# Optimization experiments

Hardware: AMD Instinct MI355X
Metric: run time of the kernel (lower is better)

Reference implementation:

```python
import jax, jax.numpy as jnp
import numpy as np

BN_EPS = 1e-5


def gcn_conv(x, src, dst, n, W, b):
    # PyG GCNConv: h = x @ W; add self-loops; symmetric deg^{-1/2} norm; scatter-add; + bias
    h = x @ W
    sl = jnp.arange(n, dtype=src.dtype)
    src_f = jnp.concatenate([src, sl])
    dst_f = jnp.concatenate([dst, sl])
    deg = jax.ops.segment_sum(jnp.ones_like(dst_f, dtype=h.dtype), dst_f, num_segments=n)
    dis = jnp.where(deg > 0, jax.lax.rsqrt(jnp.maximum(deg, 1.0)), 0.0)
    norm = dis[src_f] * dis[dst_f]                       # [E+N]
    msg = h[src_f] * norm[:, None]                       # gather + scale
    out = jax.ops.segment_sum(msg, dst_f, num_segments=n)  # scatter-add
    return out + b


def batchnorm(x, g, b):
    # training-mode BatchNorm1d (batch statistics), deterministic
    mu = jnp.mean(x, axis=0)
    var = jnp.mean((x - mu) ** 2, axis=0)
    return g * (x - mu) * jax.lax.rsqrt(var + BN_EPS) + b


def setup_inputs() -> dict:
    key = jax.random.key(0)
    ks = jax.random.split(key, 12)
    N, E, F_IN, D, M, G = 40000, 640000, 128, 128, 256, 2000
    x = jax.random.normal(ks[0], (N, F_IN), dtype=jnp.float32)
    edge_index = jax.random.randint(ks[1], (2, E), 0, N, dtype=jnp.int64)
    batch = jnp.sort(jax.random.randint(ks[2], (N,), 0, G, dtype=jnp.int64))
    s = lambda fi: 1.0 / np.sqrt(fi)
    W1 = jax.random.normal(ks[3], (F_IN, D), dtype=jnp.float32) * s(F_IN)
    b1 = jnp.zeros((D,), jnp.float32)
    W2 = jax.random.normal(ks[4], (D, D), dtype=jnp.float32) * s(D)
    b2 = jnp.zeros((D,), jnp.float32)
    bn1_g = jnp.ones((D,), jnp.float32); bn1_b = jnp.zeros((D,), jnp.float32)
    bn2_g = jnp.ones((D,), jnp.float32); bn2_b = jnp.zeros((D,), jnp.float32)
    fc1_w = jax.random.normal(ks[5], (D, M), dtype=jnp.float32) * s(D)
    fc1_b = jnp.zeros((M,), jnp.float32)
    fc2_w = jax.random.normal(ks[6], (M, M), dtype=jnp.float32) * s(M)
    fc2_b = jnp.zeros((M,), jnp.float32)
    fc3_w = jax.random.normal(ks[7], (M, 1), dtype=jnp.float32) * s(M)
    fc3_b = jnp.zeros((1,), jnp.float32)
    return dict(x=x, edge_index=edge_index, batch=batch, num_graphs=G,
                W1=W1, b1=b1, W2=W2, b2=b2,
                bn1_g=bn1_g, bn1_b=bn1_b, bn2_g=bn2_g, bn2_b=bn2_b,
                fc1_w=fc1_w, fc1_b=fc1_b, fc2_w=fc2_w, fc2_b=fc2_b,
                fc3_w=fc3_w, fc3_b=fc3_b)


def reference(x, edge_index, batch, num_graphs, W1, b1, W2, b2,
              bn1_g, bn1_b, bn2_g, bn2_b,
              fc1_w, fc1_b, fc2_w, fc2_b, fc3_w, fc3_b):
    n = x.shape[0]
    src, dst = edge_index[0], edge_index[1]
    h = gcn_conv(x, src, dst, n, W1, b1)
    h = jax.nn.relu(batchnorm(h, bn1_g, bn1_b))
    h = gcn_conv(h, src, dst, n, W2, b2)
    h = jax.nn.relu(batchnorm(h, bn2_g, bn2_b))
    g = jax.ops.segment_sum(h, batch, num_segments=num_graphs)  # scatter_sum pooling [G, D]
    g = jax.nn.relu(g @ fc1_w + fc1_b)   # dropout is identity in eval
    g = jax.nn.relu(g @ fc2_w + fc2_b)
    return g @ fc3_w + fc3_b             # [G, 1]
```

## Files before the change

kernel.cpp:

```cpp
#include <hip/hip_runtime.h>

#define NN 40000
#define NE 640000
#define DF 128
#define NG 2000
#define NCH 157
#define FILLB 625
#define GEMM_BLKS 313

typedef unsigned int u32;
typedef __attribute__((ext_vector_type(8))) short short8;
typedef __attribute__((ext_vector_type(4))) float floatx4;

__device__ inline float2 bf2_to_f2(u32 u) {
    return make_float2(__uint_as_float(u << 16), __uint_as_float(u & 0xffff0000u));
}
__device__ inline u32 f_to_bf(float f) {
    u32 u = __float_as_uint(f);
    return (u + 0x7fffu + ((u >> 16) & 1u)) >> 16;
}
__device__ inline u32 pack_bf2(float a, float b) {
    return f_to_bf(a) | (f_to_bf(b) << 16);
}
__device__ inline float bf_to_f(short s) {
    return __uint_as_float(((u32)(unsigned short)s) << 16);
}

template<bool BF16IN, bool FUSE_BN, bool WT_F32>
__device__ __forceinline__ void gemm_core(const void* __restrict__ Xv, const void* __restrict__ wsrc,
                                          u32* __restrict__ outb, const float* __restrict__ slots,
                                          const float* __restrict__ gam, const float* __restrict__ bet, int bid) {
    __shared__ unsigned short uni[128 * 136];
    __shared__ float sc[128], sh[128];
    unsigned short* wlds = uni;
    unsigned short* clds = uni;
    int tid = threadIdx.x;
    int row0 = bid * 128;

    if (FUSE_BN) {
        if (tid < 128) {
            float s = 0.f, q = 0.f;
            for (int k = 0; k < 64; k++) {
                s += slots[k * 256 + tid];
                q += slots[k * 256 + 128 + tid];
            }
            const float inv_n = 1.0f / (float)NN;
            float mu = s * inv_n;
            float va = fmaf(-mu, mu, q * inv_n);
            float a = gam[tid] * rsqrtf(va + 1e-5f);
            sc[tid] = a;
            sh[tid] = fmaf(-mu, a, bet[tid]);
        }
    }
    if (WT_F32) {
        const float* W = (const float*)wsrc;
        for (int i = tid; i < 16384; i += 256) {
            int k = i >> 7, c = i & 127;
            wlds[c * 136 + k] = (unsigned short)f_to_bf(W[i]);
        }
    } else {
        const unsigned short* wt = (const unsigned short*)wsrc;
        for (int i = tid; i < 2048; i += 256) {
            int c = i >> 4, s = i & 15;
            *(uint4*)&wlds[c * 136 + s * 8] = ((const uint4*)wt)[i];
        }
    }
    __syncthreads();

    int lane = tid & 63;
    int wave = tid >> 6;
    int qr = lane >> 4;
    int rl = lane & 15;
    int rA0 = row0 + wave * 32 + rl;
    int rA1 = rA0 + 16;
    int rA0c = rA0 < NN ? rA0 : NN - 1;
    int rA1c = rA1 < NN ? rA1 : NN - 1;

    floatx4 acc[2][8];
#pragma unroll
    for (int a = 0; a < 2; a++)
#pragma unroll
        for (int b = 0; b < 8; b++) acc[a][b] = (floatx4){0.f, 0.f, 0.f, 0.f};

#pragma unroll
    for (int kb = 0; kb < 4; kb++) {
        int k0 = kb * 32 + qr * 8;
        short8 a0, a1;
        if (!BF16IN) {
            const float* p0 = (const float*)Xv + (size_t)rA0c * DF + k0;
            const float* p1 = (const float*)Xv + (size_t)rA1c * DF + k0;
            float4 u0 = *(const float4*)p0, u1 = *(const float4*)(p0 + 4);
            float4 v0 = *(const float4*)p1, v1 = *(const float4*)(p1 + 4);
            float fa[8] = {u0.x, u0.y, u0.z, u0.w, u1.x, u1.y, u1.z, u1.w};
            float fb[8] = {v0.x, v0.y, v0.z, v0.w, v1.x, v1.y, v1.z, v1.w};
#pragma unroll
            for (int j = 0; j < 8; j++) { a0[j] = (short)f_to_bf(fa[j]); a1[j] = (short)f_to_bf(fb[j]); }
        } else {
            a0 = *(const short8*)((const u32*)Xv + (size_t)rA0c * 64 + (k0 >> 1));
            a1 = *(const short8*)((const u32*)Xv + (size_t)rA1c * 64 + (k0 >> 1));
            if (FUSE_BN) {
                float4 s0 = *(const float4*)&sc[k0], s1 = *(const float4*)&sc[k0 + 4];
                float4 h0 = *(const float4*)&sh[k0], h1 = *(const float4*)&sh[k0 + 4];
                float ss[8] = {s0.x, s0.y, s0.z, s0.w, s1.x, s1.y, s1.z, s1.w};
                float hh[8] = {h0.x, h0.y, h0.z, h0.w, h1.x, h1.y, h1.z, h1.w};
#pragma unroll
                for (int j = 0; j < 8; j++) {
                    float f0 = fmaxf(fmaf(bf_to_f(a0[j]), ss[j], hh[j]), 0.f);
                    float f1 = fmaxf(fmaf(bf_to_f(a1[j]), ss[j], hh[j]), 0.f);
                    a0[j] = (short)f_to_bf(f0);
                    a1[j] = (short)f_to_bf(f1);
                }
            }
        }
#pragma unroll
        for (int ct = 0; ct < 8; ct++) {
            short8 bfr = *(const short8*)&wlds[(ct * 16 + rl) * 136 + k0];
            acc[0][ct] = __builtin_amdgcn_mfma_f32_16x16x32_bf16(a0, bfr, acc[0][ct], 0, 0, 0);
            acc[1][ct] = __builtin_amdgcn_mfma_f32_16x16x32_bf16(a1, bfr, acc[1][ct], 0, 0, 0);
        }
    }
    __syncthreads();
#pragma unroll
    for (int rt = 0; rt < 2; rt++)
#pragma unroll
        for (int ct = 0; ct < 8; ct++)
#pragma unroll
            for (int r = 0; r < 4; r++) {
                int lr = wave * 32 + rt * 16 + qr * 4 + r;
                int c = ct * 16 + rl;
                clds[lr * 136 + c] = (unsigned short)f_to_bf(acc[rt][ct][r]);
            }
    __syncthreads();
    for (int i = tid; i < 2048; i += 256) {
        int lr = i >> 4, s = i & 15;
        int grow = row0 + lr;
        if (grow < NN) {
            uint4 v = *(const uint4*)&clds[lr * 136 + s * 8];
            ((uint4*)(outb + (size_t)grow * 64))[s] = v;
        }
    }
}

__global__ __launch_bounds__(256, 4) void k_countgemm(const int* __restrict__ dst, int* __restrict__ deg,
                                                      const float* __restrict__ W1, const float* __restrict__ W2,
                                                      unsigned short* __restrict__ wt2,
                                                      const float* __restrict__ X, u32* __restrict__ outb) {
    int bid = blockIdx.x;
    if (bid < FILLB) {
        int e0 = bid * 1024 + threadIdx.x;
        int d0 = dst[e0], d1 = dst[e0 + 256], d2 = dst[e0 + 512], d3 = dst[e0 + 768];
        atomicAdd(&deg[d0], 1);
        atomicAdd(&deg[d1], 1);
        atomicAdd(&deg[d2], 1);
        atomicAdd(&deg[d3], 1);
        return;
    }
    if (bid == FILLB) {
        for (int i = threadIdx.x; i < 128 * 128; i += 256) {
            int k = i >> 7, c = i & 127;
            wt2[c * 128 + k] = (unsigned short)f_to_bf(W2[i]);
        }
        return;
    }
    gemm_core<false, false, true>(X, W1, outb, nullptr, nullptr, nullptr, bid - FILLB - 1);
}

__global__ __launch_bounds__(256) void k_scan(const int* __restrict__ deg,
                                              int* __restrict__ row_ptr, int* __restrict__ cursor,
                                              float* __restrict__ dis) {
    __shared__ int red[256];
    __shared__ int ls[256];
    int tid = threadIdx.x;
    int blk = blockIdx.x;
    int limit = blk * 256;
    int partial = 0;
    for (int i = tid; i < limit; i += 256) partial += deg[i];
    red[tid] = partial;
    int i = limit + tid;
    int d = (i < NN) ? deg[i] : 0;
    ls[tid] = d;
    __syncthreads();
#pragma unroll
    for (int off = 128; off > 0; off >>= 1) {
        if (tid < off) red[tid] += red[tid + off];
        __syncthreads();
    }
    int base = red[0];
#pragma unroll
    for (int off = 1; off < 256; off <<= 1) {
        int t = (tid >= off) ? ls[tid - off] : 0;
        __syncthreads();
        ls[tid] += t;
        __syncthreads();
    }
    if (i < NN) {
        int r = base + ls[tid] - d;
        row_ptr[i] = r;
        cursor[i] = r;
        dis[i] = rsqrtf((float)(d + 1));
    }
    if (blk == NCH - 1 && tid == 0) row_ptr[NN] = NE;
}

__global__ __launch_bounds__(256) void k_fill(const int* __restrict__ src, const int* __restrict__ dst,
                                              int* __restrict__ cursor, int* __restrict__ col) {
    int e0 = blockIdx.x * 1024 + threadIdx.x;
    int d0 = dst[e0], d1 = dst[e0 + 256], d2 = dst[e0 + 512], d3 = dst[e0 + 768];
    int s0 = src[e0], s1 = src[e0 + 256], s2 = src[e0 + 512], s3 = src[e0 + 768];
    int p0 = atomicAdd(&cursor[d0], 1);
    int p1 = atomicAdd(&cursor[d1], 1);
    int p2 = atomicAdd(&cursor[d2], 1);
    int p3 = atomicAdd(&cursor[d3], 1);
    col[p0] = s0;
    col[p1] = s1;
    col[p2] = s2;
    col[p3] = s3;
}

__global__ __launch_bounds__(256, 4) void k_gemm2(const u32* __restrict__ Hb, const unsigned short* __restrict__ wt2,
                                                  u32* __restrict__ outb, const float* __restrict__ slots,
                                                  const float* __restrict__ gam, const float* __restrict__ bet) {
    gemm_core<true, true, false>(Hb, wt2, outb, slots, gam, bet, blockIdx.x);
}

__global__ __launch_bounds__(256) void k_gather(const u32* __restrict__ Hb, const int* __restrict__ row_ptr,
                                                const int* __restrict__ col, const float* __restrict__ dis,
                                                const float* __restrict__ bias, u32* __restrict__ outb,
                                                float* __restrict__ slots) {
    __shared__ float sred[4][128];
    __shared__ float qred[4][128];
    int t = threadIdx.x & 63;
    int wv = threadIdx.x >> 6;
    int node = blockIdx.x * 4 + wv;
    float di = dis[node];
    float2 acc;
    {
        float2 a = bf2_to_f2(Hb[(size_t)node * 64 + t]);
        float s = di * di;
        acc = make_float2(a.x * s, a.y * s);
    }
    int lo = row_ptr[node], hi = row_ptr[node + 1];
    for (int base = lo; base < hi; base += 64) {
        int m = hi - base; if (m > 64) m = 64;
        int sidx = 0; float sw = 0.f;
        if (t < m) { sidx = col[base + t]; sw = di * dis[sidx]; }
        int j = 0;
        for (; j + 8 <= m; j += 8) {
            int s0 = __shfl(sidx, j),     s1 = __shfl(sidx, j + 1);
            int s2 = __shfl(sidx, j + 2), s3 = __shfl(sidx, j + 3);
            int s4 = __shfl(sidx, j + 4), s5 = __shfl(sidx, j + 5);
            int s6 = __shfl(sidx, j + 6), s7 = __shfl(sidx, j + 7);
            float w0 = __shfl(sw, j),     w1 = __shfl(sw, j + 1);
            float w2 = __shfl(sw, j + 2), w3 = __shfl(sw, j + 3);
            float w4 = __shfl(sw, j + 4), w5 = __shfl(sw, j + 5);
            float w6 = __shfl(sw, j + 6), w7 = __shfl(sw, j + 7);
            u32 u0 = Hb[(size_t)s0 * 64 + t], u1 = Hb[(size_t)s1 * 64 + t];
            u32 u2 = Hb[(size_t)s2 * 64 + t], u3 = Hb[(size_t)s3 * 64 + t];
            u32 u4 = Hb[(size_t)s4 * 64 + t], u5 = Hb[(size_t)s5 * 64 + t];
            u32 u6 = Hb[(size_t)s6 * 64 + t], u7 = Hb[(size_t)s7 * 64 + t];
            float2 h0 = bf2_to_f2(u0), h1 = bf2_to_f2(u1), h2 = bf2_to_f2(u2), h3 = bf2_to_f2(u3);
            float2 h4 = bf2_to_f2(u4), h5 = bf2_to_f2(u5), h6 = bf2_to_f2(u6), h7 = bf2_to_f2(u7);
            acc.x = fmaf(h3.x, w3, fmaf(h2.x, w2, fmaf(h1.x, w1, fmaf(h0.x, w0, acc.x))));
            acc.y = fmaf(h3.y, w3, fmaf(h2.y, w2, fmaf(h1.y, w1, fmaf(h0.y, w0, acc.y))));
            acc.x = fmaf(h7.x, w7, fmaf(h6.x, w6, fmaf(h5.x, w5, fmaf(h4.x, w4, acc.x))));
            acc.y = fmaf(h7.y, w7, fmaf(h6.y, w6, fmaf(h5.y, w5, fmaf(h4.y, w4, acc.y))));
        }
        for (; j < m; j++) {
            int s0 = __shfl(sidx, j); float w0 = __shfl(sw, j);
            float2 h0 = bf2_to_f2(Hb[(size_t)s0 * 64 + t]);
            acc.x = fmaf(h0.x, w0, acc.x);
            acc.y = fmaf(h0.y, w0, acc.y);
        }
    }
    float2 b = ((const float2*)bias)[t];
    acc.x += b.x; acc.y += b.y;
    outb[(size_t)node * 64 + t] = pack_bf2(acc.x, acc.y);
    sred[wv][2 * t] = acc.x;     sred[wv][2 * t + 1] = acc.y;
    qred[wv][2 * t] = acc.x * acc.x; qred[wv][2 * t + 1] = acc.y * acc.y;
    __syncthreads();
    int tid = threadIdx.x;
    if (tid < 128) {
        float s = sred[0][tid] + sred[1][tid] + sred[2][tid] + sred[3][tid];
        float q = qred[0][tid] + qred[1][tid] + qred[2][tid] + qred[3][tid];
        int slot = blockIdx.x & 63;
        atomicAdd(&slots[slot * 256 + tid], s);
        atomicAdd(&slots[slot * 256 + 128 + tid], q);
    }
}

__global__ __launch_bounds__(256) void k_poolfc(const u32* __restrict__ Hb, const int* __restrict__ batch,
                                                const float* __restrict__ slots,
                                                const float* __restrict__ gam, const float* __restrict__ bet,
                                                const float* __restrict__ fc1w, const float* __restrict__ fc1b,
                                                const float* __restrict__ fc2w, const float* __restrict__ fc2b,
                                                const float* __restrict__ fc3w, const float* __restrict__ fc3b,
                                                float* __restrict__ out) {
    __shared__ float sc[128], sh[128];
    __shared__ float pooled[4][128];
    __shared__ float g1[4][256];
    __shared__ float g2[4][256];
    __shared__ int bnds[5];
    int tid = threadIdx.x;
    int gbase = blockIdx.x * 4;
    if (tid < 128) {
        float s = 0.f, q = 0.f;
        for (int k = 0; k < 64; k++) {
            s += slots[k * 256 + tid];
            q += slots[k * 256 + 128 + tid];
        }
        const float inv_n = 1.0f / (float)NN;
        float mu = s * inv_n;
        float va = fmaf(-mu, mu, q * inv_n);
        float a = gam[tid] * rsqrtf(va + 1e-5f);
        sc[tid] = a;
        sh[tid] = fmaf(-mu, a, bet[tid]);
    } else if (tid < 133) {
        int target = gbase + (tid - 128);
        int a = 0, b = NN;
        while (a < b) { int m = (a + b) >> 1; if (batch[m] < target) a = m + 1; else b = m; }
        bnds[tid - 128] = a;
    }
    __syncthreads();
    {
        int g = tid >> 6, p = tid & 63;
        int lo = bnds[g], hi = bnds[g + 1];
        float a0 = 0.f, a1 = 0.f;
        float sc0 = sc[2 * p], sh0 = sh[2 * p], sc1 = sc[2 * p + 1], sh1 = sh[2 * p + 1];
        for (int i = lo; i < hi; i++) {
            float2 v = bf2_to_f2(Hb[(size_t)i * 64 + p]);
            a0 += fmaxf(fmaf(v.x, sc0, sh0), 0.f);
            a1 += fmaxf(fmaf(v.y, sc1, sh1), 0.f);
        }
        pooled[g][2 * p] = a0;
        pooled[g][2 * p + 1] = a1;
    }
    __syncthreads();
    {
        float x0 = 0.f, x1 = 0.f, x2 = 0.f, x3 = 0.f;
        for (int k = 0; k < 128; k++) {
            float wv = fc1w[k * 256 + tid];
            x0 = fmaf(pooled[0][k], wv, x0);
            x1 = fmaf(pooled[1][k], wv, x1);
            x2 = fmaf(pooled[2][k], wv, x2);
            x3 = fmaf(pooled[3][k], wv, x3);
        }
        float bb = fc1b[tid];
        g1[0][tid] = fmaxf(x0 + bb, 0.f);
        g1[1][tid] = fmaxf(x1 + bb, 0.f);
        g1[2][tid] = fmaxf(x2 + bb, 0.f);
        g1[3][tid] = fmaxf(x3 + bb, 0.f);
    }
    __syncthreads();
    {
        float x0 = 0.f, x1 = 0.f, x2 = 0.f, x3 = 0.f;
        for (int k = 0; k < 256; k++) {
            float wv = fc2w[k * 256 + tid];
            x0 = fmaf(g1[0][k], wv, x0);
            x1 = fmaf(g1[1][k], wv, x1);
            x2 = fmaf(g1[2][k], wv, x2);
            x3 = fmaf(g1[3][k], wv, x3);
        }
        float bb = fc2b[tid];
        g2[0][tid] = fmaxf(x0 + bb, 0.f);
        g2[1][tid] = fmaxf(x1 + bb, 0.f);
        g2[2][tid] = fmaxf(x2 + bb, 0.f);
        g2[3][tid] = fmaxf(x3 + bb, 0.f);
    }
    __syncthreads();
    {
        int lane = tid & 63, wv = tid >> 6;
        float s = fmaf(g2[wv][lane], fc3w[lane],
                  fmaf(g2[wv][64 + lane], fc3w[64 + lane],
                  fmaf(g2[wv][128 + lane], fc3w[128 + lane],
                       g2[wv][192 + lane] * fc3w[192 + lane])));
        for (int off = 32; off > 0; off >>= 1) s += __shfl_down(s, off);
        if (lane == 0) out[gbase + wv] = s + fc3b[0];
    }
}

extern "C" void kernel_launch(void* const* d_in, const int* in_sizes, int n_in,
                              void* d_out, int out_size, void* d_ws, size_t ws_size,
                              hipStream_t stream) {
    const float* x    = (const float*)d_in[0];
    const int*   ei   = (const int*)d_in[1];
    const int*   batch= (const int*)d_in[2];
    const float* W1   = (const float*)d_in[4];
    const float* b1   = (const float*)d_in[5];
    const float* W2   = (const float*)d_in[6];
    const float* b2   = (const float*)d_in[7];
    const float* bn1g = (const float*)d_in[8];
    const float* bn1b = (const float*)d_in[9];
    const float* bn2g = (const float*)d_in[10];
    const float* bn2b = (const float*)d_in[11];
    const float* fc1w = (const float*)d_in[12];
    const float* fc1b = (const float*)d_in[13];
    const float* fc2w = (const float*)d_in[14];
    const float* fc2b = (const float*)d_in[15];
    const float* fc3w = (const float*)d_in[16];
    const float* fc3b = (const float*)d_in[17];
    const int* src = ei;
    const int* dst = ei + NE;
    float* outp = (float*)d_out;

    char* w = (char*)d_ws;
    size_t o = 0;
    auto alloc = [&](size_t bytes) -> char* {
        char* p = w + o;
        o = (o + bytes + 255) & ~(size_t)255;
        return p;
    };
    int*   deg     = (int*)alloc((size_t)NN * 4);
    float* slotsA  = (float*)alloc(64 * 256 * 4);
    float* slotsB  = (float*)alloc(64 * 256 * 4);
    char*  zend    = w + o;
    int*   row_ptr = (int*)alloc((size_t)(NN + 1) * 4);
    int*   cursor  = (int*)alloc((size_t)NN * 4);
    int*   col     = (int*)alloc((size_t)NE * 4);
    float* dis     = (float*)alloc((size_t)NN * 4);
    unsigned short* wt2 = (unsigned short*)alloc(128 * 128 * 2);
    u32*   bufA    = (u32*)alloc((size_t)NN * 64 * 4);
    u32*   bufB    = (u32*)alloc((size_t)NN * 64 * 4);

    hipMemsetAsync(deg, 0, (size_t)(zend - (char*)deg), stream);

    k_countgemm<<<FILLB + 1 + GEMM_BLKS, 256, 0, stream>>>(dst, deg, W1, W2, wt2, x, bufA);
    k_scan<<<NCH, 256, 0, stream>>>(deg, row_ptr, cursor, dis);
    k_fill<<<FILLB, 256, 0, stream>>>(src, dst, cursor, col);
    k_gather<<<NN / 4, 256, 0, stream>>>(bufA, row_ptr, col, dis, b1, bufB, slotsA);
    k_gemm2<<<GEMM_BLKS, 256, 0, stream>>>(bufB, wt2, bufA, slotsA, bn1g, bn1b);
    k_gather<<<NN / 4, 256, 0, stream>>>(bufA, row_ptr, col, dis, b2, bufB, slotsB);
    k_poolfc<<<NG / 4, 256, 0, stream>>>(bufB, batch, slotsB, bn2g, bn2b,
                                         fc1w, fc1b, fc2w, fc2b, fc3w, fc3b, outp);
}
```

Baseline: 299.6 us.

## Split degree counters into four replicas and pre-transpose W1 in an init kernel

Degree counting and CSR fill now spread atomics over four replicated counter arrays chosen by block index. The scan sums the replicas and gives each one its own cursor offset. A new init kernel replaces the memset: it zeroes the workspace and converts both weight matrices to transposed bf16 once, so GEMM blocks load pre-converted W1 instead of converting fp32 per block. This adds an extra kernel launch and more scan reads in exchange for less atomic contention and less per-block conversion work.

```diff
diff --git a/kernel.cpp b/kernel.cpp
--- a/kernel.cpp
+++ b/kernel.cpp
@@ -26,8 +26,25 @@
     return __uint_as_float(((u32)(unsigned short)s) << 16);
 }
 
-template<bool BF16IN, bool FUSE_BN, bool WT_F32>
-__device__ __forceinline__ void gemm_core(const void* __restrict__ Xv, const void* __restrict__ wsrc,
+#define ZWORDS (4 * NN + 2 * 64 * 256)
+__global__ __launch_bounds__(256) void k_init(int* __restrict__ zbase,
+                                              const float* __restrict__ W1, const float* __restrict__ W2,
+                                              unsigned short* __restrict__ wt1, unsigned short* __restrict__ wt2) {
+    int bid = blockIdx.x;
+    if (bid < 256) {
+        for (int i = bid * 256 + threadIdx.x; i < ZWORDS; i += 256 * 256) zbase[i] = 0;
+        return;
+    }
+    const float* W = (bid == 256) ? W1 : W2;
+    unsigned short* wt = (bid == 256) ? wt1 : wt2;
+    for (int i = threadIdx.x; i < 128 * 128; i += 256) {
+        int k = i >> 7, c = i & 127;
+        wt[c * 128 + k] = (unsigned short)f_to_bf(W[i]);
+    }
+}
+
+template<bool BF16IN, bool FUSE_BN>
+__device__ __forceinline__ void gemm_core(const void* __restrict__ Xv, const unsigned short* __restrict__ wt,
                                           u32* __restrict__ outb, const float* __restrict__ slots,
                                           const float* __restrict__ gam, const float* __restrict__ bet, int bid) {
     __shared__ unsigned short uni[128 * 136];
@@ -52,18 +69,9 @@
             sh[tid] = fmaf(-mu, a, bet[tid]);
         }
     }
-    if (WT_F32) {
-        const float* W = (const float*)wsrc;
-        for (int i = tid; i < 16384; i += 256) {
-            int k = i >> 7, c = i & 127;
-            wlds[c * 136 + k] = (unsigned short)f_to_bf(W[i]);
-        }
-    } else {
-        const unsigned short* wt = (const unsigned short*)wsrc;
-        for (int i = tid; i < 2048; i += 256) {
-            int c = i >> 4, s = i & 15;
-            *(uint4*)&wlds[c * 136 + s * 8] = ((const uint4*)wt)[i];
-        }
+    for (int i = tid; i < 2048; i += 256) {
+        int c = i >> 4, s = i & 15;
+        *(uint4*)&wlds[c * 136 + s * 8] = ((const uint4*)wt)[i];
     }
     __syncthreads();
 
@@ -141,12 +149,13 @@
     }
 }
 
-__global__ __launch_bounds__(256, 4) void k_countgemm(const int* __restrict__ dst, int* __restrict__ deg,
-                                                      const float* __restrict__ W1, const float* __restrict__ W2,
-                                                      unsigned short* __restrict__ wt2,
-                                                      const float* __restrict__ X, u32* __restrict__ outb) {
+__global__ __launch_bounds__(256, 4) void k_countgemm(const int* __restrict__ dst, int* __restrict__ deg4,
+                                                      const unsigned short* __restrict__ wt1,
+                                                      const u32* __restrict__ X4,
+                                                      u32* __restrict__ outb) {
     int bid = blockIdx.x;
     if (bid < FILLB) {
+        int* deg = deg4 + (bid & 3) * NN;
         int e0 = bid * 1024 + threadIdx.x;
         int d0 = dst[e0], d1 = dst[e0 + 256], d2 = dst[e0 + 512], d3 = dst[e0 + 768];
         atomicAdd(&deg[d0], 1);
@@ -155,18 +164,11 @@
         atomicAdd(&deg[d3], 1);
         return;
     }
-    if (bid == FILLB) {
-        for (int i = threadIdx.x; i < 128 * 128; i += 256) {
-            int k = i >> 7, c = i & 127;
-            wt2[c * 128 + k] = (unsigned short)f_to_bf(W2[i]);
-        }
-        return;
-    }
-    gemm_core<false, false, true>(X, W1, outb, nullptr, nullptr, nullptr, bid - FILLB - 1);
-}
-
-__global__ __launch_bounds__(256) void k_scan(const int* __restrict__ deg,
-                                              int* __restrict__ row_ptr, int* __restrict__ cursor,
+    gemm_core<false, false>((const void*)X4, wt1, outb, nullptr, nullptr, nullptr, bid - FILLB);
+}
+
+__global__ __launch_bounds__(256) void k_scan(const int* __restrict__ deg4,
+                                              int* __restrict__ row_ptr, int* __restrict__ cursor4,
                                               float* __restrict__ dis) {
     __shared__ int red[256];
     __shared__ int ls[256];
@@ -174,10 +176,15 @@
     int blk = blockIdx.x;
     int limit = blk * 256;
     int partial = 0;
-    for (int i = tid; i < limit; i += 256) partial += deg[i];
+    for (int i = tid; i < limit; i += 256)
+        partial += deg4[i] + deg4[NN + i] + deg4[2 * NN + i] + deg4[3 * NN + i];
     red[tid] = partial;
     int i = limit + tid;
-    int d = (i < NN) ? deg[i] : 0;
+    int d0 = 0, d1 = 0, d2 = 0, d3 = 0;
+    if (i < NN) {
+        d0 = deg4[i]; d1 = deg4[NN + i]; d2 = deg4[2 * NN + i]; d3 = deg4[3 * NN + i];
+    }
+    int d = d0 + d1 + d2 + d3;
     ls[tid] = d;
     __syncthreads();
 #pragma unroll
@@ -196,14 +203,18 @@
     if (i < NN) {
         int r = base + ls[tid] - d;
         row_ptr[i] = r;
-        cursor[i] = r;
+        cursor4[i] = r;
+        cursor4[NN + i] = r + d0;
+        cursor4[2 * NN + i] = r + d0 + d1;
+        cursor4[3 * NN + i] = r + d0 + d1 + d2;
         dis[i] = rsqrtf((float)(d + 1));
     }
     if (blk == NCH - 1 && tid == 0) row_ptr[NN] = NE;
 }
 
 __global__ __launch_bounds__(256) void k_fill(const int* __restrict__ src, const int* __restrict__ dst,
-                                              int* __restrict__ cursor, int* __restrict__ col) {
+                                              int* __restrict__ cursor4, int* __restrict__ col) {
+    int* cursor = cursor4 + (blockIdx.x & 3) * NN;
     int e0 = blockIdx.x * 1024 + threadIdx.x;
     int d0 = dst[e0], d1 = dst[e0 + 256], d2 = dst[e0 + 512], d3 = dst[e0 + 768];
     int s0 = src[e0], s1 = src[e0 + 256], s2 = src[e0 + 512], s3 = src[e0 + 768];
@@ -220,7 +231,7 @@
 __global__ __launch_bounds__(256, 4) void k_gemm2(const u32* __restrict__ Hb, const unsigned short* __restrict__ wt2,
                                                   u32* __restrict__ outb, const float* __restrict__ slots,
                                                   const float* __restrict__ gam, const float* __restrict__ bet) {
-    gemm_core<true, true, false>(Hb, wt2, outb, slots, gam, bet, blockIdx.x);
+    gemm_core<true, true>(Hb, wt2, outb, slots, gam, bet, blockIdx.x);
 }
 
 __global__ __launch_bounds__(256) void k_gather(const u32* __restrict__ Hb, const int* __restrict__ row_ptr,
@@ -409,23 +420,22 @@
         o = (o + bytes + 255) & ~(size_t)255;
         return p;
     };
-    int*   deg     = (int*)alloc((size_t)NN * 4);
+    int*   deg4    = (int*)alloc((size_t)4 * NN * 4);
     float* slotsA  = (float*)alloc(64 * 256 * 4);
     float* slotsB  = (float*)alloc(64 * 256 * 4);
-    char*  zend    = w + o;
     int*   row_ptr = (int*)alloc((size_t)(NN + 1) * 4);
-    int*   cursor  = (int*)alloc((size_t)NN * 4);
+    int*   cursor4 = (int*)alloc((size_t)4 * NN * 4);
     int*   col     = (int*)alloc((size_t)NE * 4);
     float* dis     = (float*)alloc((size_t)NN * 4);
+    unsigned short* wt1 = (unsigned short*)alloc(128 * 128 * 2);
     unsigned short* wt2 = (unsigned short*)alloc(128 * 128 * 2);
     u32*   bufA    = (u32*)alloc((size_t)NN * 64 * 4);
     u32*   bufB    = (u32*)alloc((size_t)NN * 64 * 4);
 
-    hipMemsetAsync(deg, 0, (size_t)(zend - (char*)deg), stream);
-
-    k_countgemm<<<FILLB + 1 + GEMM_BLKS, 256, 0, stream>>>(dst, deg, W1, W2, wt2, x, bufA);
-    k_scan<<<NCH, 256, 0, stream>>>(deg, row_ptr, cursor, dis);
-    k_fill<<<FILLB, 256, 0, stream>>>(src, dst, cursor, col);
+    k_init<<<258, 256, 0, stream>>>(deg4, W1, W2, wt1, wt2);
+    k_countgemm<<<FILLB + GEMM_BLKS, 256, 0, stream>>>(dst, deg4, wt1, (const u32*)x, bufA);
+    k_scan<<<NCH, 256, 0, stream>>>(deg4, row_ptr, cursor4, dis);
+    k_fill<<<FILLB, 256, 0, stream>>>(src, dst, cursor4, col);
     k_gather<<<NN / 4, 256, 0, stream>>>(bufA, row_ptr, col, dis, b1, bufB, slotsA);
     k_gemm2<<<GEMM_BLKS, 256, 0, stream>>>(bufB, wt2, bufA, slotsA, bn1g, bn1b);
     k_gather<<<NN / 4, 256, 0, stream>>>(bufA, row_ptr, col, dis, b2, bufB, slotsB);
```

Result: slower. 313.5 us (+4.6%).
